# Optimization experiments

Hardware: AMD Instinct MI355X
Metric: run time of the kernel (lower is better)

Reference implementation:

```python
import jax, jax.numpy as jnp
import numpy as np

DISCOUNT_FACTOR = 0.99
AVERAGE_LAMBDA = 0.9
EPS = 1e-8
B, S = 8192, 2048


def setup_inputs() -> dict:
    key = jax.random.key(0)
    k1, k2, k3 = jax.random.split(key, 3)
    values = jax.random.normal(k1, (B, S + 1, 1), jnp.float32)
    rewards = jax.random.normal(k2, (B, S, 1), jnp.float32)
    # binary done flags stored as float, as in the torch module's math
    dones = (jax.random.uniform(k3, (B, S, 1)) < 0.02).astype(jnp.float32)
    # parameter init identical to GammaLambdaLearner.__init__ (atanh of targets)
    raw_gamma = jnp.arctanh(jnp.full((1,), DISCOUNT_FACTOR, jnp.float32))
    raw_lambd = jnp.arctanh(jnp.full((S,), AVERAGE_LAMBDA, jnp.float32))
    return {"values": values, "rewards": rewards, "dones": dones,
            "raw_gamma": raw_gamma, "raw_lambd": raw_lambd}


def reference(values, rewards, dones, raw_gamma, raw_lambd):
    # gamma / lambd properties: tanh then clamp_min(1e-8)
    gamma = jnp.maximum(jnp.tanh(raw_gamma), EPS)          # [1]
    lambd = jnp.maximum(jnp.tanh(raw_lambd), EPS)          # [S]

    # time-major views for the scan: [S, B, 1]
    r = jnp.swapaxes(rewards, 0, 1)
    d = jnp.swapaxes(dones, 0, 1)
    v_next = jnp.swapaxes(values[:, 1:], 0, 1)

    def step(carry, xs):
        # carry: lambda_return[t+1], shape [B, 1]
        r_t, d_t, vn_t, lam_t = xs
        ret = r_t + gamma * (1.0 - d_t) * ((1.0 - lam_t) * vn_t + lam_t * carry)
        return ret, ret

    # backward-in-time recurrence bootstrapped from the final value estimate
    _, outs = jax.lax.scan(step, values[:, -1], (r, d, v_next, lambd), reverse=True)
    return jnp.swapaxes(outs, 0, 1)  # [B, S, 1]
```

## Files before the change

### kernel.cpp

```cpp
#include <hip/hip_runtime.h>
#include <math.h>


#define EPSV 1e-8f

__global__ void precompute_lambda_kernel(const float* __restrict__ raw_gamma,
                                         const float* __restrict__ raw_lambd,
                                         float* __restrict__ lam, int S) {
    int t = blockIdx.x * blockDim.x + threadIdx.x;
    if (t < S) lam[t] = fmaxf(tanhf(raw_lambd[t]), EPSV);
    if (t == S) lam[S] = fmaxf(tanhf(raw_gamma[0]), EPSV);
}

__global__ __launch_bounds__(256) void lamret_kernel(
    const float* __restrict__ values,
    const float* __restrict__ rewards,
    const float* __restrict__ dones,
    const float* __restrict__ raw_gamma,
    const float* __restrict__ raw_lambd,
    const float* __restrict__ lam_pre,
    float* __restrict__ out,
    int S)
{
    constexpr int C = 8;
    const int row  = blockIdx.x;
    const int tid  = threadIdx.x;
    const int lane = tid & 63;
    const int wave = tid >> 6;
    const int nwaves = blockDim.x >> 6;
    const int t0 = tid * C;

    const float* __restrict__ rrow = rewards + (size_t)row * S;
    const float* __restrict__ drow = dones   + (size_t)row * S;
    const float* __restrict__ vrow = values  + (size_t)row * (S + 1);

    float gamma;
    if (lam_pre) gamma = lam_pre[S];
    else         gamma = fmaxf(tanhf(raw_gamma[0]), EPSV);

    float a[C], b[C];
    const bool full = (t0 + C <= S);
    if (full) {
        const float4* r4 = reinterpret_cast<const float4*>(rrow + t0);
        const float4* d4 = reinterpret_cast<const float4*>(drow + t0);
        float4 r01 = r4[0], r23 = r4[1];
        float4 d01 = d4[0], d23 = d4[1];
        float rr[C] = {r01.x, r01.y, r01.z, r01.w, r23.x, r23.y, r23.z, r23.w};
        float dd[C] = {d01.x, d01.y, d01.z, d01.w, d23.x, d23.y, d23.z, d23.w};
        float lm[C];
        if (lam_pre) {
            const float4* l4 = reinterpret_cast<const float4*>(lam_pre + t0);
            float4 l01 = l4[0], l23 = l4[1];
            lm[0]=l01.x; lm[1]=l01.y; lm[2]=l01.z; lm[3]=l01.w;
            lm[4]=l23.x; lm[5]=l23.y; lm[6]=l23.z; lm[7]=l23.w;
        } else {
            #pragma unroll
            for (int i = 0; i < C; ++i) lm[i] = fmaxf(tanhf(raw_lambd[t0 + i]), EPSV);
        }
        float vv[C];
        #pragma unroll
        for (int i = 0; i < C; ++i) vv[i] = vrow[t0 + 1 + i];
        #pragma unroll
        for (int i = 0; i < C; ++i) {
            float g1d = gamma * (1.0f - dd[i]);
            a[i] = g1d * lm[i];
            b[i] = rr[i] + g1d * (1.0f - lm[i]) * vv[i];
        }
    } else {
        #pragma unroll
        for (int i = 0; i < C; ++i) {
            int t = t0 + i;
            if (t < S) {
                float lmv = lam_pre ? lam_pre[t] : fmaxf(tanhf(raw_lambd[t]), EPSV);
                float g1d = gamma * (1.0f - drow[t]);
                a[i] = g1d * lmv;
                b[i] = rrow[t] + g1d * (1.0f - lmv) * vrow[t + 1];
            } else { a[i] = 1.0f; b[i] = 0.0f; }
        }
    }

    float A = 1.0f, Bc = 0.0f;
    #pragma unroll
    for (int i = C - 1; i >= 0; --i) {
        Bc = fmaf(a[i], Bc, b[i]);
        A  = a[i] * A;
    }

    float Ai = A, Bi = Bc;
    #pragma unroll
    for (int off = 1; off < 64; off <<= 1) {
        float Ao = __shfl_down(Ai, off);
        float Bo = __shfl_down(Bi, off);
        if (lane + off < 64) {
            Bi = fmaf(Ai, Bo, Bi);
            Ai = Ai * Ao;
        }
    }
    float Ae = __shfl_down(Ai, 1);
    float Be = __shfl_down(Bi, 1);
    if (lane == 63) { Ae = 1.0f; Be = 0.0f; }

    __shared__ float aggA[8], aggB[8];
    if (lane == 0) { aggA[wave] = Ai; aggB[wave] = Bi; }
    __syncthreads();
    float TA = 1.0f, TB = 0.0f;
    for (int w2 = wave + 1; w2 < nwaves; ++w2) {
        TB = fmaf(TA, aggB[w2], TB);
        TA = TA * aggA[w2];
    }
    float Af = Ae * TA;
    float Bf = fmaf(Ae, TB, Be);

    const float vlast = vrow[S];
    float x = fmaf(Af, vlast, Bf);

    float o[C];
    #pragma unroll
    for (int i = C - 1; i >= 0; --i) {
        x = fmaf(a[i], x, b[i]);
        o[i] = x;
    }

    float* __restrict__ orow = out + (size_t)row * S;
    if (full) {
        float4* o4 = reinterpret_cast<float4*>(orow + t0);
        o4[0] = make_float4(o[0], o[1], o[2], o[3]);
        o4[1] = make_float4(o[4], o[5], o[6], o[7]);
    } else {
        for (int i = 0; i < C; ++i)
            if (t0 + i < S) orow[t0 + i] = o[i];
    }
}

extern "C" void kernel_launch(void* const* d_in, const int* in_sizes, int n_in,
                              void* d_out, int out_size, void* d_ws, size_t ws_size,
                              hipStream_t stream) {
    const float* values    = (const float*)d_in[0];
    const float* rewards   = (const float*)d_in[1];
    const float* dones     = (const float*)d_in[2];
    const float* raw_gamma = (const float*)d_in[3];
    const float* raw_lambd = (const float*)d_in[4];
    float* out = (float*)d_out;

    const int S = in_sizes[4];
    const int B = in_sizes[1] / S;

    float* lam_pre = nullptr;
    if (ws_size >= (size_t)(S + 1) * sizeof(float)) {
        lam_pre = (float*)d_ws;
        int nthr = 256;
        int nblk = (S + 1 + nthr - 1) / nthr;
        precompute_lambda_kernel<<<nblk, nthr, 0, stream>>>(raw_gamma, raw_lambd, lam_pre, S);
    }

    lamret_kernel<<<B, 256, 0, stream>>>(values, rewards, dones,
                                         raw_gamma, raw_lambd, lam_pre, out, S);
}
```

Measured before the change: 216.3 us.

## Stage values row in padded LDS and use nontemporal loads/stores

Each block now loads its values row into padded shared memory with coalesced loads, replacing the misaligned strided per-thread reads of vrow (the row stride is S+1, so it cannot be read as float4). Rewards, dones and outputs now use nontemporal vector loads and stores to avoid polluting the cache with streaming data. This adds an extra barrier and LDS usage per block. The wave count is also hardcoded to 4, which assumes 256-thread blocks.

```diff
diff --git a/kernel.cpp b/kernel.cpp
--- a/kernel.cpp
+++ b/kernel.cpp
@@ -3,6 +3,10 @@
 
 
 #define EPSV 1e-8f
+#define MAX_S 2048
+#define LDSF(t) ((t) + ((t) >> 3))
+
+typedef float f32x4 __attribute__((ext_vector_type(4)));
 
 __global__ void precompute_lambda_kernel(const float* __restrict__ raw_gamma,
                                          const float* __restrict__ raw_lambd,
@@ -23,48 +27,71 @@
     int S)
 {
     constexpr int C = 8;
+    __shared__ float vbuf[LDSF(MAX_S) + 2];
+    __shared__ float aggA[4], aggB[4];
+
     const int row  = blockIdx.x;
     const int tid  = threadIdx.x;
     const int lane = tid & 63;
     const int wave = tid >> 6;
-    const int nwaves = blockDim.x >> 6;
+    const int nwaves = 4;
     const int t0 = tid * C;
 
     const float* __restrict__ rrow = rewards + (size_t)row * S;
     const float* __restrict__ drow = dones   + (size_t)row * S;
     const float* __restrict__ vrow = values  + (size_t)row * (S + 1);
 
+    const bool use_lds = (S <= MAX_S);
+    if (use_lds) {
+        for (int t = tid; t <= S; t += 256)
+            vbuf[LDSF(t)] = __builtin_nontemporal_load(vrow + t);
+    }
+
     float gamma;
     if (lam_pre) gamma = lam_pre[S];
     else         gamma = fmaxf(tanhf(raw_gamma[0]), EPSV);
 
     float a[C], b[C];
-    const bool full = (t0 + C <= S);
+    const bool full = (t0 + C <= S) && ((S & 3) == 0);
+    float rr[C], dd[C], lm[C];
     if (full) {
-        const float4* r4 = reinterpret_cast<const float4*>(rrow + t0);
-        const float4* d4 = reinterpret_cast<const float4*>(drow + t0);
-        float4 r01 = r4[0], r23 = r4[1];
-        float4 d01 = d4[0], d23 = d4[1];
-        float rr[C] = {r01.x, r01.y, r01.z, r01.w, r23.x, r23.y, r23.z, r23.w};
-        float dd[C] = {d01.x, d01.y, d01.z, d01.w, d23.x, d23.y, d23.z, d23.w};
-        float lm[C];
+        const f32x4* r4 = reinterpret_cast<const f32x4*>(rrow + t0);
+        const f32x4* d4 = reinterpret_cast<const f32x4*>(drow + t0);
+        f32x4 r01 = __builtin_nontemporal_load(r4);
+        f32x4 r23 = __builtin_nontemporal_load(r4 + 1);
+        f32x4 d01 = __builtin_nontemporal_load(d4);
+        f32x4 d23 = __builtin_nontemporal_load(d4 + 1);
+        #pragma unroll
+        for (int i = 0; i < 4; ++i) { rr[i] = r01[i]; rr[4+i] = r23[i]; }
+        #pragma unroll
+        for (int i = 0; i < 4; ++i) { dd[i] = d01[i]; dd[4+i] = d23[i]; }
         if (lam_pre) {
-            const float4* l4 = reinterpret_cast<const float4*>(lam_pre + t0);
-            float4 l01 = l4[0], l23 = l4[1];
-            lm[0]=l01.x; lm[1]=l01.y; lm[2]=l01.z; lm[3]=l01.w;
-            lm[4]=l23.x; lm[5]=l23.y; lm[6]=l23.z; lm[7]=l23.w;
+            const f32x4* l4 = reinterpret_cast<const f32x4*>(lam_pre + t0);
+            f32x4 l01 = l4[0], l23 = l4[1];
+            #pragma unroll
+            for (int i = 0; i < 4; ++i) { lm[i] = l01[i]; lm[4+i] = l23[i]; }
         } else {
             #pragma unroll
             for (int i = 0; i < C; ++i) lm[i] = fmaxf(tanhf(raw_lambd[t0 + i]), EPSV);
         }
+    }
+
+    if (use_lds) __syncthreads();
+
+    if (full) {
         float vv[C];
-        #pragma unroll
-        for (int i = 0; i < C; ++i) vv[i] = vrow[t0 + 1 + i];
+        if (use_lds) {
+            #pragma unroll
+            for (int i = 0; i < C; ++i) { int t = t0 + 1 + i; vv[i] = vbuf[LDSF(t)]; }
+        } else {
+            #pragma unroll
+            for (int i = 0; i < C; ++i) vv[i] = vrow[t0 + 1 + i];
+        }
         #pragma unroll
         for (int i = 0; i < C; ++i) {
             float g1d = gamma * (1.0f - dd[i]);
             a[i] = g1d * lm[i];
-            b[i] = rr[i] + g1d * (1.0f - lm[i]) * vv[i];
+            b[i] = fmaf(g1d * (1.0f - lm[i]), vv[i], rr[i]);
         }
     } else {
         #pragma unroll
@@ -73,8 +100,9 @@
             if (t < S) {
                 float lmv = lam_pre ? lam_pre[t] : fmaxf(tanhf(raw_lambd[t]), EPSV);
                 float g1d = gamma * (1.0f - drow[t]);
+                float vnt = use_lds ? vbuf[LDSF(t + 1)] : vrow[t + 1];
                 a[i] = g1d * lmv;
-                b[i] = rrow[t] + g1d * (1.0f - lmv) * vrow[t + 1];
+                b[i] = fmaf(g1d * (1.0f - lmv), vnt, rrow[t]);
             } else { a[i] = 1.0f; b[i] = 0.0f; }
         }
     }
@@ -100,7 +128,6 @@
     float Be = __shfl_down(Bi, 1);
     if (lane == 63) { Ae = 1.0f; Be = 0.0f; }
 
-    __shared__ float aggA[8], aggB[8];
     if (lane == 0) { aggA[wave] = Ai; aggB[wave] = Bi; }
     __syncthreads();
     float TA = 1.0f, TB = 0.0f;
@@ -111,7 +138,7 @@
     float Af = Ae * TA;
     float Bf = fmaf(Ae, TB, Be);
 
-    const float vlast = vrow[S];
+    const float vlast = use_lds ? vbuf[LDSF(S)] : vrow[S];
     float x = fmaf(Af, vlast, Bf);
 
     float o[C];
@@ -123,9 +150,12 @@
 
     float* __restrict__ orow = out + (size_t)row * S;
     if (full) {
-        float4* o4 = reinterpret_cast<float4*>(orow + t0);
-        o4[0] = make_float4(o[0], o[1], o[2], o[3]);
-        o4[1] = make_float4(o[4], o[5], o[6], o[7]);
+        f32x4* o4 = reinterpret_cast<f32x4*>(orow + t0);
+        f32x4 o01, o23;
+        #pragma unroll
+        for (int i = 0; i < 4; ++i) { o01[i] = o[i]; o23[i] = o[4+i]; }
+        __builtin_nontemporal_store(o01, o4);
+        __builtin_nontemporal_store(o23, o4 + 1);
     } else {
         for (int i = 0; i < C; ++i)
             if (t0 + i < S) orow[t0 + i] = o[i];
```

Result: no change. 215.2 us (-0.5%).
